# Kernel tuning notes

Hardware: AMD Instinct MI355X
Metric: run time of the kernel (lower is better)

The kernel has to match this reference:

```python
import jax, jax.numpy as jnp
import numpy as np

Cin, E, L, M, H, Cout = 256, 16, 64, 64, 64, 256
B, N = 16, 2048
D = M + L * E  # hypernetwork input dim = 1088


def setup_inputs() -> dict:
    key = jax.random.key(0)
    ks = jax.random.split(key, 8)
    def lin(k, fan_in, shape):
        return jax.random.normal(k, shape, jnp.float32) / np.float32(np.sqrt(fan_in))
    return {
        "x0": jax.random.randint(ks[0], (B, N), 0, Cin),
        "emb": jax.random.normal(ks[1], (Cin, E), jnp.float32) * 0.02,
        "W_enc_w": lin(ks[2], D, (D, H)), "W_enc_b": jnp.zeros((H,), jnp.float32),
        "W_dec_w": lin(ks[3], H, (H, M * M)), "W_dec_b": jnp.zeros((M * M,), jnp.float32),
        "b_enc_w": lin(ks[4], D, (D, H)), "b_enc_b": jnp.zeros((H,), jnp.float32),
        "b_dec_w": lin(ks[5], H, (H, M)), "b_dec_b": jnp.zeros((M,), jnp.float32),
        "dec_w": lin(ks[6], M, (M, Cout)), "dec_b": jnp.zeros((Cout,), jnp.float32),
    }


def reference(x0, emb, W_enc_w, W_enc_b, W_dec_w, W_dec_b,
              b_enc_w, b_enc_b, b_dec_w, b_dec_b, dec_w, dec_b):
    Bq, Nq = x0.shape
    inv_ln2 = jnp.float32(1.0 / np.log(2.0))
    # left-pad with token id 0 (torch pad on int indices pads zeros -> embedding row 0)
    xp = jnp.concatenate([jnp.zeros((Bq, L), x0.dtype), x0], axis=-1)  # [B, N+L]
    e = emb[xp]  # [B, N+L, E]
    # window for step t = tokens t-L..t-1 of x0 = xp[:, t:t+L]
    idxs = jnp.arange(Nq)[:, None] + jnp.arange(L)[None, :]  # [N, L]
    win = e[:, idxs].reshape(Bq, Nq, L * E).transpose(1, 0, 2)  # [N, B, L*E]
    ys = x0.T  # [N, B]

    def mlp(x, ew, eb, dw, db):
        return jax.nn.sigmoid(x @ ew + eb) @ dw + db

    def step(m, xy):
        w, y = xy  # w: [B, L*E], y: [B]
        inp = jnp.concatenate([m, w], axis=-1)  # [B, M + L*E]
        Wm = mlp(inp, W_enc_w, W_enc_b, W_dec_w, W_dec_b).reshape(Bq, M, M)
        bm = mlp(inp, b_enc_w, b_enc_b, b_dec_w, b_dec_b)  # [B, M]
        m = jax.nn.sigmoid(jnp.einsum('bij,bj->bi', Wm, m) + bm)
        logits = m @ dec_w + dec_b  # [B, Cout]
        lse = jax.nn.log_softmax(logits)
        loss = -jnp.take_along_axis(lse, y[:, None], axis=1)[:, 0] * inv_ln2
        return m, loss

    m0 = jnp.zeros((Bq, M), jnp.float32)
    _, losses = jax.lax.scan(step, m0, (win, ys))  # losses: [N, B]
    return losses.reshape(-1)  # matches torch.cat(losses): time-major [N*B]
```

## Files before the change

### kernel.cpp

```cpp
#include <hip/hip_runtime.h>
#include <hip/hip_bf16.h>
#include <hip/hip_fp16.h>


typedef unsigned int uint_t;
typedef unsigned short us_t;
typedef unsigned long long u64_t;
typedef _Float16 h2_t __attribute__((ext_vector_type(2)));

__device__ __forceinline__ us_t f2bf(float f) {
    uint_t u = __float_as_uint(f);
    uint_t r = u + 0x7fffu + ((u >> 16) & 1u);
    return (us_t)(r >> 16);
}
__device__ __forceinline__ float bflo(uint_t u) { return __uint_as_float(u << 16); }
__device__ __forceinline__ float bfhi(uint_t u) { return __uint_as_float(u & 0xffff0000u); }

__device__ __forceinline__ us_t f2h(float f) {
    __half h = __float2half(f);
    return *reinterpret_cast<us_t*>(&h);
}
__device__ __forceinline__ float h2f(us_t s) {
    __half h = *reinterpret_cast<__half*>(&s);
    return __half2float(h);
}
__device__ __forceinline__ h2_t u2h2(uint_t u) {
    union { uint_t u; h2_t h; } x; x.u = u; return x.h;
}

#if __has_builtin(__builtin_amdgcn_fdot2)
__device__ __forceinline__ float dot2f(uint_t a, uint_t b, float c) {
    return __builtin_amdgcn_fdot2(u2h2(a), u2h2(b), c, false);
}
#else
__device__ __forceinline__ float dot2f(uint_t a, uint_t b, float c) {
    h2_t x = u2h2(a), y = u2h2(b);
    return c + (float)x.x * (float)y.x + (float)x.y * (float)y.y;
}
#endif

#define DOT4(q, base, acc)                                              \
    acc = dot2f(q.x, mreg2u[(base) + 0], acc);                          \
    acc = dot2f(q.y, mreg2u[(base) + 1], acc);                          \
    acc = dot2f(q.z, mreg2u[(base) + 2], acc);                          \
    acc = dot2f(q.w, mreg2u[(base) + 3], acc);

__global__ void cvt_kernel(const float* __restrict__ Wdecw,
                           const float* __restrict__ decw,
                           const float* __restrict__ Wencw,
                           const float* __restrict__ bencw,
                           us_t* __restrict__ WdG, us_t* __restrict__ decwY,
                           us_t* __restrict__ EWmG) {
    int o = blockIdx.x * 256 + threadIdx.x;
    if (o < 262144) {
        int s = o >> 16;
        int idx = o & 65535;
        int k = idx & 7;
        int oo = (idx >> 3) & 1023;
        int jp = idx >> 13;
        int h = s * 16 + (oo >> 6);
        int i = oo & 63;
        int j = jp * 8 + k;
        WdG[o] = f2h(Wdecw[h * 4096 + i * 64 + j]);
    } else if (o < 278528) {
        int oo = o - 262144;
        int k = oo & 3, lane = (oo >> 2) & 63, mm = oo >> 8;
        decwY[oo] = f2bf(decw[mm * 256 + k * 64 + lane]);
    } else if (o < 286720) {
        int oo = o - 278528;
        int kk = oo & 7, h2 = (oo >> 3) & 127, jp = oo >> 10;
        int j = jp * 8 + kk;
        float v = (h2 < 64) ? Wencw[j * 64 + h2] : bencw[j * 64 + (h2 - 64)];
        EWmG[oo] = f2h(v);
    }
}

__global__ void build_T(const float* __restrict__ emb, const float* __restrict__ Wencw,
                        const float* __restrict__ bencw, float* __restrict__ T) {
    int l = blockIdx.x >> 8, v = blockIdx.x & 255, h2 = threadIdx.x;
    float acc = 0.f;
#pragma unroll
    for (int e = 0; e < 16; ++e) {
        int d = 64 + l * 16 + e;
        float w = (h2 < 64) ? Wencw[d * 64 + h2] : bencw[d * 64 + (h2 - 64)];
        acc += emb[v * 16 + e] * w;
    }
    T[blockIdx.x * 128 + h2] = acc;
}

__global__ void build_P(const float* __restrict__ T, const int* __restrict__ x0,
                        const float* __restrict__ Wencb, const float* __restrict__ bencb,
                        float* __restrict__ P) {
    int t = blockIdx.x >> 4, b = blockIdx.x & 15, h2 = threadIdx.x;
    float acc = (h2 < 64) ? Wencb[h2] : bencb[h2 - 64];
    for (int l = 0; l < 64; ++l) {
        int p = t + l;
        int v = (p < 64) ? 0 : x0[b * 2048 + (p - 64)];
        acc += T[(l * 256 + v) * 128 + h2];
    }
    P[blockIdx.x * 128 + h2] = acc;
}

__global__ __launch_bounds__(512, 2) void recur(
    const float* __restrict__ bdecw, const float* __restrict__ bdecb,
    const float* __restrict__ Wdecb, const us_t* __restrict__ WdG,
    const us_t* __restrict__ EWmG, const float* __restrict__ P,
    uint_t* __restrict__ mh32, u64_t* __restrict__ pxb) {
    const int b = blockIdx.x & 15, s = blockIdx.x >> 4;
    const int tid = threadIdx.x;

    extern __shared__ char smem[];
    us_t*   EWm2   = (us_t*)(smem);
    uint_t* wdbt2  = (uint_t*)(smem + 16384);
    uint_t* bdec2  = (uint_t*)(smem + 24576);
    float*  V_s    = (float*)(smem + 32768);
    float*  rp4_s  = (float*)(smem + 36928);
    float*  wdbm2_s= (float*)(smem + 37952);
    float*  hbb2_s = (float*)(smem + 38464);
    float*  hw_s   = (float*)(smem + 38976);
    uint_t* hb2_s  = (uint_t*)(smem + 39232);
    uint_t* m2_s   = (uint_t*)(smem + 39360);
    float*  bias_s = (float*)(smem + 39488);

    uint4 wreg[16];
    {
        const uint4* g4 = (const uint4*)WdG + s * 8192;
#pragma unroll
        for (int jp = 0; jp < 8; ++jp) {
            wreg[jp]     = g4[jp * 1024 + tid];
            wreg[8 + jp] = g4[jp * 1024 + tid + 512];
        }
    }
    {
        const uint4* g4 = (const uint4*)EWmG;
        uint4* l4 = (uint4*)EWm2;
        for (int k = tid; k < 1024; k += 512) l4[k] = g4[k];
    }
    for (int k = tid; k < 2048; k += 512) {
        int jj = k >> 6, i = k & 63;
        wdbt2[k] = (uint_t)f2h(Wdecb[i * 64 + 2 * jj])
                 | ((uint_t)f2h(Wdecb[i * 64 + 2 * jj + 1]) << 16);
        bdec2[k] = (uint_t)f2h(bdecw[(2 * jj) * 64 + i])
                 | ((uint_t)f2h(bdecw[(2 * jj + 1) * 64 + i]) << 16);
    }
    if (tid < 64) bias_s[tid] = bdecb[tid];
    if (tid < 32) m2_s[tid] = 0u;
    __syncthreads();

    uint_t mreg2u[32];
#pragma unroll
    for (int j = 0; j < 32; ++j) mreg2u[j] = 0u;

    float preg = 0.f;
    if (tid < 128) preg = P[b * 128 + tid];

    const uint4* EW4 = (const uint4*)EWm2;
    const int hl = tid >> 6, iA = tid & 63;
    const int w = tid >> 6;

    for (int t = 0; t < 2048; ++t) {
        float pnext = 0.f;
        int tp = (t < 2047) ? (t + 1) : 2047;
        if (tid < 128) pnext = P[(tp * 16 + b) * 128 + tid];

        float a0 = 0.f, a1 = 0.f;
#pragma unroll
        for (int jp = 0; jp < 8; ++jp) {
            uint4 q0 = wreg[jp];
            uint4 q1 = wreg[8 + jp];
            DOT4(q0, jp * 4, a0);
            DOT4(q1, jp * 4, a1);
        }
        V_s[hl * 65 + iA] = a0;
        V_s[(hl + 8) * 65 + iA] = a1;

        if (tid < 128) {
            float acc = preg;
#pragma unroll
            for (int jp = 0; jp < 8; ++jp) {
                uint4 e = EW4[jp * 128 + tid];
                DOT4(e, jp * 4, acc);
            }
            float sg = 1.f / (1.f + __expf(-acc));
            if (tid < 64) {
                hw_s[tid] = sg;
            } else {
                int l = tid - 64;
                float vlo = __shfl(sg, (l & 31) * 2, 64);
                float vhi = __shfl(sg, (l & 31) * 2 + 1, 64);
                if (l < 32)
                    hb2_s[l] = (uint_t)f2h(vlo) | ((uint_t)f2h(vhi) << 16);
            }
        }
        preg = pnext;
        __syncthreads();

        u64_t* slotb = pxb + (u64_t)(((t & 1) * 16 + b) * 4) * 64;
        const uint_t tg = (uint_t)(t + 1);

        if (tid < 64) {
            float r0 = 0.f, r1 = 0.f;
#pragma unroll
            for (int hh = 0; hh < 8; ++hh) {
                r0 += hw_s[s * 16 + 2 * hh]     * V_s[(2 * hh) * 65 + tid];
                r1 += hw_s[s * 16 + 2 * hh + 1] * V_s[(2 * hh + 1) * 65 + tid];
            }
            float rs = r0 + r1;
            rp4_s[s * 64 + tid] = rs;
            u64_t pay = ((u64_t)tg << 32) | (u64_t)__float_as_uint(rs);
            __hip_atomic_store(slotb + s * 64 + tid, pay,
                               __ATOMIC_RELAXED, __HIP_MEMORY_SCOPE_AGENT);
        }

        if (w < 3) {
            int p = w + (w >= s ? 1 : 0);
            int lane = tid & 63;
            const u64_t* src = slotb + p * 64 + lane;
            u64_t v;
            for (;;) {
                v = __hip_atomic_load(src, __ATOMIC_RELAXED,
                                      __HIP_MEMORY_SCOPE_AGENT);
                if (__ballot((uint_t)(v >> 32) == tg) == ~0ull) break;
                __builtin_amdgcn_s_sleep(1);
            }
            rp4_s[p * 64 + lane] = __uint_as_float((uint_t)v);
        } else if (w < 5) {
            int i = tid & 63;
            float wm = 0.f, hbv = 0.f;
            if (w == 3) {
#pragma unroll
                for (int jj = 0; jj < 16; ++jj) {
                    wm  = dot2f(wdbt2[jj * 64 + i], mreg2u[jj], wm);
                    hbv = dot2f(bdec2[jj * 64 + i], hb2_s[jj], hbv);
                }
                wdbm2_s[i] = wm;
                hbb2_s[i] = hbv;
            } else {
#pragma unroll
                for (int jj = 0; jj < 16; ++jj) {
                    wm  = dot2f(wdbt2[(16 + jj) * 64 + i], mreg2u[16 + jj], wm);
                    hbv = dot2f(bdec2[(16 + jj) * 64 + i], hb2_s[16 + jj], hbv);
                }
                wdbm2_s[64 + i] = wm;
                hbb2_s[64 + i] = hbv;
            }
        }
        __syncthreads();

        if (tid < 64) {
            float r = ((rp4_s[tid] + rp4_s[64 + tid])
                     + (rp4_s[128 + tid] + rp4_s[192 + tid]))
                    + (wdbm2_s[tid] + wdbm2_s[64 + tid])
                    + (hbb2_s[tid] + hbb2_s[64 + tid])
                    + bias_s[tid];
            float nm = 1.f / (1.f + __expf(-r));
            us_t nh = f2h(nm);
            uint_t nhu = (uint_t)nh;
            uint_t lo = (uint_t)__shfl((int)nhu, (tid & 31) * 2, 64);
            uint_t hi = (uint_t)__shfl((int)nhu, (tid & 31) * 2 + 1, 64);
            if (tid < 32) {
                uint_t pk = lo | (hi << 16);
                m2_s[tid] = pk;
                if (s == 0) mh32[(t * 16 + b) * 32 + tid] = pk;
            }
        }
        __syncthreads();

        {
            const uint4* mg = (const uint4*)m2_s;
#pragma unroll
            for (int p = 0; p < 8; ++p) {
                uint4 v = mg[p];
                mreg2u[p * 4 + 0] = v.x;
                mreg2u[p * 4 + 1] = v.y;
                mreg2u[p * 4 + 2] = v.z;
                mreg2u[p * 4 + 3] = v.w;
            }
        }
    }
}

__global__ __launch_bounds__(256) void loss_kernel(
    const us_t* __restrict__ mhb, const us_t* __restrict__ decwY,
    const float* __restrict__ decb, const int* __restrict__ x0,
    float* __restrict__ out) {
    __shared__ __align__(16) us_t dw[16384];
    const int tid = threadIdx.x;
    {
        const uint4* g4 = (const uint4*)decwY;
        uint4* l4 = (uint4*)dw;
        for (int k = tid; k < 2048; k += 256) l4[k] = g4[k];
    }
    __syncthreads();
    const int lane = tid & 63, wv = tid >> 6;
    const uint2* dwu2 = (const uint2*)dw;
    float b0 = decb[lane], b1 = decb[lane + 64];
    float b2 = decb[lane + 128], b3 = decb[lane + 192];
    for (int r = 0; r < 8; ++r) {
        int row = blockIdx.x * 32 + wv * 8 + r;
        float mL = h2f(mhb[row * 64 + lane]);
        float l0 = b0, l1 = b1, l2 = b2, l3 = b3;
#pragma unroll
        for (int mm = 0; mm < 64; ++mm) {
            float mv = __shfl(mL, mm, 64);
            uint2 q = dwu2[mm * 64 + lane];
            l0 += mv * bflo(q.x);
            l1 += mv * bfhi(q.x);
            l2 += mv * bflo(q.y);
            l3 += mv * bfhi(q.y);
        }
        float mx = fmaxf(fmaxf(l0, l1), fmaxf(l2, l3));
#pragma unroll
        for (int o = 32; o > 0; o >>= 1) mx = fmaxf(mx, __shfl_xor(mx, o, 64));
        float se = __expf(l0 - mx) + __expf(l1 - mx) + __expf(l2 - mx) + __expf(l3 - mx);
#pragma unroll
        for (int o = 32; o > 0; o >>= 1) se += __shfl_xor(se, o, 64);
        float lse = mx + __logf(se);
        int t = row >> 4, bb = row & 15;
        int y = x0[bb * 2048 + t];
        int hi = y >> 6;
        float cand = hi == 0 ? l0 : (hi == 1 ? l1 : (hi == 2 ? l2 : l3));
        float ly = __shfl(cand, y & 63, 64);
        if (lane == 0) out[row] = (lse - ly) * 1.4426950408889634f;
    }
}

extern "C" void kernel_launch(void* const* d_in, const int* in_sizes, int n_in,
                              void* d_out, int out_size, void* d_ws, size_t ws_size,
                              hipStream_t stream) {
    const int*   x0    = (const int*)d_in[0];
    const float* emb   = (const float*)d_in[1];
    const float* Wencw = (const float*)d_in[2];
    const float* Wencb = (const float*)d_in[3];
    const float* Wdecw = (const float*)d_in[4];
    const float* Wdecb = (const float*)d_in[5];
    const float* bencw = (const float*)d_in[6];
    const float* bencb = (const float*)d_in[7];
    const float* bdecw = (const float*)d_in[8];
    const float* bdecb = (const float*)d_in[9];
    const float* decw  = (const float*)d_in[10];
    const float* decb  = (const float*)d_in[11];
    float* out = (float*)d_out;

    char* ws = (char*)d_ws;
    us_t*   WdG   = (us_t*)(ws);
    us_t*   decwY = (us_t*)(ws + 524288);
    us_t*   EWmG  = (us_t*)(ws + 557056);
    u64_t*  pxb   = (u64_t*)(ws + 573440);
    float*  T     = (float*)(ws + 638976);
    uint_t* mh32  = (uint_t*)T;
    float*  P     = (float*)(ws + 9027584);

    static const int kRecurLds = 157632;
    (void)hipFuncSetAttribute((const void*)recur,
                              hipFuncAttributeMaxDynamicSharedMemorySize,
                              kRecurLds);

    cvt_kernel<<<1120, 256, 0, stream>>>(Wdecw, decw, Wencw, bencw,
                                         WdG, decwY, EWmG);
    build_T<<<16384, 128, 0, stream>>>(emb, Wencw, bencw, T);
    build_P<<<32768, 128, 0, stream>>>(T, x0, Wencb, bencb, P);
    (void)hipMemsetAsync(pxb, 0, 65536, stream);
    recur<<<64, 512, kRecurLds, stream>>>(bdecw, bdecb, Wdecb, WdG, EWmG,
                                          P, mh32, pxb);
    loss_kernel<<<1024, 256, 0, stream>>>((const us_t*)mh32, decwY, decb, x0, out);
}
```

Before: 3.722 ms.

## Run each batch recurrence in one block instead of four cooperating blocks

The recurrence kernel now uses one 512-thread block per batch element instead of four blocks that split the hidden dimension and exchanged partial sums through global-memory flag polling. Each block now handles all 64 hidden units: a quarter of the decoder weights stays in registers, a quarter sits in LDS, and the other half is streamed from global/L2 every timestep. This removes the cross-block spin-wait synchronisation and the memset it needed. In exchange each block does four times the per-step matvec work and adds heavy per-step global weight traffic, using only 16 CUs.

```diff
diff --git a/kernel.cpp b/kernel.cpp
--- a/kernel.cpp
+++ b/kernel.cpp
@@ -53,14 +53,13 @@
                            us_t* __restrict__ EWmG) {
     int o = blockIdx.x * 256 + threadIdx.x;
     if (o < 262144) {
-        int s = o >> 16;
-        int idx = o & 65535;
-        int k = idx & 7;
-        int oo = (idx >> 3) & 1023;
-        int jp = idx >> 13;
-        int h = s * 16 + (oo >> 6);
-        int i = oo & 63;
-        int j = jp * 8 + k;
+        int kk = o & 7;
+        int tid = (o >> 3) & 511;
+        int jp = (o >> 12) & 7;
+        int c = o >> 15;
+        int h = c * 8 + (tid >> 6);
+        int i = tid & 63;
+        int j = jp * 8 + kk;
         WdG[o] = f2h(Wdecw[h * 4096 + i * 64 + j]);
     } else if (o < 278528) {
         int oo = o - 262144;
@@ -105,43 +104,46 @@
     const float* __restrict__ bdecw, const float* __restrict__ bdecb,
     const float* __restrict__ Wdecb, const us_t* __restrict__ WdG,
     const us_t* __restrict__ EWmG, const float* __restrict__ P,
-    uint_t* __restrict__ mh32, u64_t* __restrict__ pxb) {
-    const int b = blockIdx.x & 15, s = blockIdx.x >> 4;
+    uint_t* __restrict__ mh32) {
+    const int b = blockIdx.x;
     const int tid = threadIdx.x;
+    const int i = tid & 63, q = tid >> 6;
 
     extern __shared__ char smem[];
-    us_t*   EWm2   = (us_t*)(smem);
-    uint_t* wdbt2  = (uint_t*)(smem + 16384);
-    uint_t* bdec2  = (uint_t*)(smem + 24576);
-    float*  V_s    = (float*)(smem + 32768);
-    float*  rp4_s  = (float*)(smem + 36928);
-    float*  wdbm2_s= (float*)(smem + 37952);
-    float*  hbb2_s = (float*)(smem + 38464);
-    float*  hw_s   = (float*)(smem + 38976);
-    uint_t* hb2_s  = (uint_t*)(smem + 39232);
-    uint_t* m2_s   = (uint_t*)(smem + 39360);
-    float*  bias_s = (float*)(smem + 39488);
+    float*  V_s    = (float*)(smem);
+    float*  rp8_s  = (float*)(smem + 16384);
+    float*  wmhb_s = (float*)(smem + 18432);
+    float*  hw_s   = (float*)(smem + 20480);
+    uint_t* hb2_s  = (uint_t*)(smem + 20736);
+    uint_t* m2_s   = (uint_t*)(smem + 20864);
+    float*  bias_s = (float*)(smem + 20992);
+    us_t*   Wd_lds = (us_t*)(smem + 21248);
+
+    const uint4* g4 = (const uint4*)WdG;
+    const uint4* EW4 = (const uint4*)EWmG;
 
     uint4 wreg[16];
+#pragma unroll
+    for (int jp = 0; jp < 8; ++jp) {
+        wreg[jp]     = g4[jp * 512 + tid];
+        wreg[8 + jp] = g4[(8 + jp) * 512 + tid];
+    }
     {
-        const uint4* g4 = (const uint4*)WdG + s * 8192;
+        uint4* l4w = (uint4*)Wd_lds;
 #pragma unroll
         for (int jp = 0; jp < 8; ++jp) {
-            wreg[jp]     = g4[jp * 1024 + tid];
-            wreg[8 + jp] = g4[jp * 1024 + tid + 512];
-        }
-    }
-    {
-        const uint4* g4 = (const uint4*)EWmG;
-        uint4* l4 = (uint4*)EWm2;
-        for (int k = tid; k < 1024; k += 512) l4[k] = g4[k];
-    }
-    for (int k = tid; k < 2048; k += 512) {
-        int jj = k >> 6, i = k & 63;
-        wdbt2[k] = (uint_t)f2h(Wdecb[i * 64 + 2 * jj])
-                 | ((uint_t)f2h(Wdecb[i * 64 + 2 * jj + 1]) << 16);
-        bdec2[k] = (uint_t)f2h(bdecw[(2 * jj) * 64 + i])
-                 | ((uint_t)f2h(bdecw[(2 * jj + 1) * 64 + i]) << 16);
+            l4w[jp * 512 + tid]       = g4[(16 + jp) * 512 + tid];
+            l4w[(8 + jp) * 512 + tid] = g4[(24 + jp) * 512 + tid];
+        }
+    }
+    uint_t wdbtreg[4], bdecreg[4];
+#pragma unroll
+    for (int k = 0; k < 4; ++k) {
+        int jj = q * 4 + k;
+        wdbtreg[k] = (uint_t)f2h(Wdecb[i * 64 + 2 * jj])
+                   | ((uint_t)f2h(Wdecb[i * 64 + 2 * jj + 1]) << 16);
+        bdecreg[k] = (uint_t)f2h(bdecw[(2 * jj) * 64 + i])
+                   | ((uint_t)f2h(bdecw[(2 * jj + 1) * 64 + i]) << 16);
     }
     if (tid < 64) bias_s[tid] = bdecb[tid];
     if (tid < 32) m2_s[tid] = 0u;
@@ -154,33 +156,58 @@
     float preg = 0.f;
     if (tid < 128) preg = P[b * 128 + tid];
 
-    const uint4* EW4 = (const uint4*)EWm2;
-    const int hl = tid >> 6, iA = tid & 63;
-    const int w = tid >> 6;
+    const uint4* l4 = (const uint4*)Wd_lds;
 
     for (int t = 0; t < 2048; ++t) {
         float pnext = 0.f;
         int tp = (t < 2047) ? (t + 1) : 2047;
         if (tid < 128) pnext = P[(tp * 16 + b) * 128 + tid];
 
-        float a0 = 0.f, a1 = 0.f;
-#pragma unroll
-        for (int jp = 0; jp < 8; ++jp) {
-            uint4 q0 = wreg[jp];
-            uint4 q1 = wreg[8 + jp];
-            DOT4(q0, jp * 4, a0);
-            DOT4(q1, jp * 4, a1);
-        }
-        V_s[hl * 65 + iA] = a0;
-        V_s[(hl + 8) * 65 + iA] = a1;
+        uint4 sA[8], sB[8], eS[8];
+#pragma unroll
+        for (int jp = 0; jp < 8; ++jp) sA[jp] = g4[(32 + jp) * 512 + tid];
+#pragma unroll
+        for (int jp = 0; jp < 8; ++jp) sB[jp] = g4[(40 + jp) * 512 + tid];
+        if (tid < 128) {
+#pragma unroll
+            for (int jp = 0; jp < 8; ++jp) eS[jp] = EW4[jp * 128 + tid];
+        }
+
+        float a0 = 0, a1 = 0, a2 = 0, a3 = 0, a4 = 0, a5 = 0, a6 = 0, a7 = 0;
+#pragma unroll
+        for (int jp = 0; jp < 8; ++jp) { uint4 v = wreg[jp];     DOT4(v, jp * 4, a0); }
+#pragma unroll
+        for (int jp = 0; jp < 8; ++jp) { uint4 v = wreg[8 + jp]; DOT4(v, jp * 4, a1); }
+#pragma unroll
+        for (int jp = 0; jp < 8; ++jp) { uint4 v = l4[jp * 512 + tid];       DOT4(v, jp * 4, a2); }
+#pragma unroll
+        for (int jp = 0; jp < 8; ++jp) { uint4 v = l4[(8 + jp) * 512 + tid]; DOT4(v, jp * 4, a3); }
+#pragma unroll
+        for (int jp = 0; jp < 8; ++jp) { DOT4(sA[jp], jp * 4, a4); }
+#pragma unroll
+        for (int jp = 0; jp < 8; ++jp) sA[jp] = g4[(48 + jp) * 512 + tid];
+#pragma unroll
+        for (int jp = 0; jp < 8; ++jp) { DOT4(sB[jp], jp * 4, a5); }
+#pragma unroll
+        for (int jp = 0; jp < 8; ++jp) sB[jp] = g4[(56 + jp) * 512 + tid];
+#pragma unroll
+        for (int jp = 0; jp < 8; ++jp) { DOT4(sA[jp], jp * 4, a6); }
+#pragma unroll
+        for (int jp = 0; jp < 8; ++jp) { DOT4(sB[jp], jp * 4, a7); }
+
+        V_s[tid]        = a0;
+        V_s[512 + tid]  = a1;
+        V_s[1024 + tid] = a2;
+        V_s[1536 + tid] = a3;
+        V_s[2048 + tid] = a4;
+        V_s[2560 + tid] = a5;
+        V_s[3072 + tid] = a6;
+        V_s[3584 + tid] = a7;
 
         if (tid < 128) {
             float acc = preg;
 #pragma unroll
-            for (int jp = 0; jp < 8; ++jp) {
-                uint4 e = EW4[jp * 128 + tid];
-                DOT4(e, jp * 4, acc);
-            }
+            for (int jp = 0; jp < 8; ++jp) { DOT4(eS[jp], jp * 4, acc); }
             float sg = 1.f / (1.f + __expf(-acc));
             if (tid < 64) {
                 hw_s[tid] = sg;
@@ -195,64 +222,28 @@
         preg = pnext;
         __syncthreads();
 
-        u64_t* slotb = pxb + (u64_t)(((t & 1) * 16 + b) * 4) * 64;
-        const uint_t tg = (uint_t)(t + 1);
+        {
+            float r = 0.f;
+#pragma unroll
+            for (int hh = 0; hh < 8; ++hh)
+                r += hw_s[q * 8 + hh] * V_s[(q * 8 + hh) * 64 + i];
+            rp8_s[q * 64 + i] = r;
+            float wh = 0.f;
+#pragma unroll
+            for (int k = 0; k < 4; ++k) {
+                wh = dot2f(wdbtreg[k], m2_s[q * 4 + k], wh);
+                wh = dot2f(bdecreg[k], hb2_s[q * 4 + k], wh);
+            }
+            wmhb_s[q * 64 + i] = wh;
+        }
+        __syncthreads();
 
         if (tid < 64) {
-            float r0 = 0.f, r1 = 0.f;
-#pragma unroll
-            for (int hh = 0; hh < 8; ++hh) {
-                r0 += hw_s[s * 16 + 2 * hh]     * V_s[(2 * hh) * 65 + tid];
-                r1 += hw_s[s * 16 + 2 * hh + 1] * V_s[(2 * hh + 1) * 65 + tid];
-            }
-            float rs = r0 + r1;
-            rp4_s[s * 64 + tid] = rs;
-            u64_t pay = ((u64_t)tg << 32) | (u64_t)__float_as_uint(rs);
-            __hip_atomic_store(slotb + s * 64 + tid, pay,
-                               __ATOMIC_RELAXED, __HIP_MEMORY_SCOPE_AGENT);
-        }
-
-        if (w < 3) {
-            int p = w + (w >= s ? 1 : 0);
-            int lane = tid & 63;
-            const u64_t* src = slotb + p * 64 + lane;
-            u64_t v;
-            for (;;) {
-                v = __hip_atomic_load(src, __ATOMIC_RELAXED,
-                                      __HIP_MEMORY_SCOPE_AGENT);
-                if (__ballot((uint_t)(v >> 32) == tg) == ~0ull) break;
-                __builtin_amdgcn_s_sleep(1);
-            }
-            rp4_s[p * 64 + lane] = __uint_as_float((uint_t)v);
-        } else if (w < 5) {
-            int i = tid & 63;
-            float wm = 0.f, hbv = 0.f;
-            if (w == 3) {
-#pragma unroll
-                for (int jj = 0; jj < 16; ++jj) {
-                    wm  = dot2f(wdbt2[jj * 64 + i], mreg2u[jj], wm);
-                    hbv = dot2f(bdec2[jj * 64 + i], hb2_s[jj], hbv);
-                }
-                wdbm2_s[i] = wm;
-                hbb2_s[i] = hbv;
-            } else {
-#pragma unroll
-                for (int jj = 0; jj < 16; ++jj) {
-                    wm  = dot2f(wdbt2[(16 + jj) * 64 + i], mreg2u[16 + jj], wm);
-                    hbv = dot2f(bdec2[(16 + jj) * 64 + i], hb2_s[16 + jj], hbv);
-                }
-                wdbm2_s[64 + i] = wm;
-                hbb2_s[64 + i] = hbv;
-            }
-        }
-        __syncthreads();
-
-        if (tid < 64) {
-            float r = ((rp4_s[tid] + rp4_s[64 + tid])
-                     + (rp4_s[128 + tid] + rp4_s[192 + tid]))
-                    + (wdbm2_s[tid] + wdbm2_s[64 + tid])
-                    + (hbb2_s[tid] + hbb2_s[64 + tid])
-                    + bias_s[tid];
+            float r = bias_s[tid];
+#pragma unroll
+            for (int qq = 0; qq < 8; ++qq) r += rp8_s[qq * 64 + tid];
+#pragma unroll
+            for (int qq = 0; qq < 8; ++qq) r += wmhb_s[qq * 64 + tid];
             float nm = 1.f / (1.f + __expf(-r));
             us_t nh = f2h(nm);
             uint_t nhu = (uint_t)nh;
@@ -261,7 +252,7 @@
             if (tid < 32) {
                 uint_t pk = lo | (hi << 16);
                 m2_s[tid] = pk;
-                if (s == 0) mh32[(t * 16 + b) * 32 + tid] = pk;
+                mh32[(t * 16 + b) * 32 + tid] = pk;
             }
         }
         __syncthreads();
@@ -303,11 +294,11 @@
 #pragma unroll
         for (int mm = 0; mm < 64; ++mm) {
             float mv = __shfl(mL, mm, 64);
-            uint2 q = dwu2[mm * 64 + lane];
-            l0 += mv * bflo(q.x);
-            l1 += mv * bfhi(q.x);
-            l2 += mv * bflo(q.y);
-            l3 += mv * bfhi(q.y);
+            uint2 qq = dwu2[mm * 64 + lane];
+            l0 += mv * bflo(qq.x);
+            l1 += mv * bfhi(qq.x);
+            l2 += mv * bflo(qq.y);
+            l3 += mv * bfhi(qq.y);
         }
         float mx = fmaxf(fmaxf(l0, l1), fmaxf(l2, l3));
 #pragma unroll
@@ -346,12 +337,11 @@
     us_t*   WdG   = (us_t*)(ws);
     us_t*   decwY = (us_t*)(ws + 524288);
     us_t*   EWmG  = (us_t*)(ws + 557056);
-    u64_t*  pxb   = (u64_t*)(ws + 573440);
-    float*  T     = (float*)(ws + 638976);
+    float*  T     = (float*)(ws + 573440);
     uint_t* mh32  = (uint_t*)T;
-    float*  P     = (float*)(ws + 9027584);
-
-    static const int kRecurLds = 157632;
+    float*  P     = (float*)(ws + 8962048);
+
+    static const int kRecurLds = 152320;
     (void)hipFuncSetAttribute((const void*)recur,
                               hipFuncAttributeMaxDynamicSharedMemorySize,
                               kRecurLds);
@@ -360,8 +350,7 @@
                                          WdG, decwY, EWmG);
     build_T<<<16384, 128, 0, stream>>>(emb, Wencw, bencw, T);
     build_P<<<32768, 128, 0, stream>>>(T, x0, Wencb, bencb, P);
-    (void)hipMemsetAsync(pxb, 0, 65536, stream);
-    recur<<<64, 512, kRecurLds, stream>>>(bdecw, bdecb, Wdecb, WdG, EWmG,
-                                          P, mh32, pxb);
+    recur<<<16, 512, kRecurLds, stream>>>(bdecw, bdecb, Wdecb, WdG, EWmG,
+                                          P, mh32);
     loss_kernel<<<1024, 256, 0, stream>>>((const us_t*)mh32, decwY, decb, x0, out);
 }
```

Result: slower. 10.33 ms (+177.6%).
